# Kernel tuning notes

Measured on AMD Instinct MI355X. Metric: run time of the kernel, lower is better.

The kernel has to match this reference:

```python
import jax, jax.numpy as jnp
import numpy as np

B, N, K = 4, 4096, 16
D_POINTS, D_MODEL = 64, 256


def _ln(x, g, b, eps=1e-5):
    mu = jnp.mean(x, axis=-1, keepdims=True)
    var = jnp.mean((x - mu) ** 2, axis=-1, keepdims=True)
    return (x - mu) * jax.lax.rsqrt(var + eps) * g + b


def _gather(points, idx):
    # points: [B,N,C], idx: [B,N,K] -> [B,N,K,C]
    b = jnp.arange(points.shape[0])[:, None, None]
    return points[b, idx]


def setup_inputs() -> dict:
    key = jax.random.key(0)
    ks = jax.random.split(key, 16)
    std_qkv = np.sqrt(2.0 / D_MODEL).astype(np.float32)
    return {
        "xyz": jax.random.normal(ks[0], (B, N, 3), jnp.float32),
        "features": jax.random.normal(ks[1], (B, N, D_POINTS), jnp.float32),
        "W_pre": jax.random.normal(ks[2], (D_MODEL, D_POINTS), jnp.float32) * 0.02,
        "b_pre": jnp.zeros((D_MODEL,), jnp.float32),
        "W_post": jax.random.normal(ks[3], (D_POINTS, D_MODEL), jnp.float32) * 0.02,
        "b_post": jnp.zeros((D_POINTS,), jnp.float32),
        "Wp1": jax.random.normal(ks[4], (D_MODEL, 3), jnp.float32) * 0.02,
        "Wp2": jax.random.normal(ks[5], (D_MODEL, D_MODEL), jnp.float32) * 0.02,
        "Wa1": jax.random.normal(ks[6], (D_MODEL, D_MODEL), jnp.float32) * 0.02,
        "Wa2": jax.random.normal(ks[7], (D_MODEL, D_MODEL), jnp.float32) * 0.02,
        "WQ": jax.random.normal(ks[8], (D_MODEL, D_MODEL), jnp.float32) * std_qkv,
        "WK": jax.random.normal(ks[9], (D_MODEL, D_MODEL), jnp.float32) * std_qkv,
        "WV": jax.random.normal(ks[10], (D_MODEL, D_MODEL), jnp.float32) * std_qkv,
        "Wproj": jax.random.normal(ks[11], (D_MODEL, D_MODEL), jnp.float32) * 0.02,
        "g_dm": jnp.ones((D_MODEL,), jnp.float32),
        "b_dm": jnp.zeros((D_MODEL,), jnp.float32),
        "g_dp": jnp.ones((D_POINTS,), jnp.float32),
        "b_dp": jnp.zeros((D_POINTS,), jnp.float32),
    }


def reference(xyz, features, W_pre, b_pre, W_post, b_post, Wp1, Wp2, Wa1, Wa2,
              WQ, WK, WV, Wproj, g_dm, b_dm, g_dp, b_dp):
    # kNN (state == 'l'): pairwise squared distances, k smallest per point
    dists = jnp.sum((xyz[:, :, None, :] - xyz[:, None, :, :]) ** 2, axis=-1)  # [B,N,N]
    _, idx = jax.lax.top_k(-dists, K)  # [B,N,K] smallest distances (incl. self)

    knn_xyz = _gather(xyz, idx)                      # [B,N,K,3]
    inp = features @ W_pre.T + b_pre                 # [B,N,D]

    q = _ln(inp @ WQ.T, g_dm, b_dm)                  # [B,N,D]
    k_ = _gather(_ln(inp @ WK.T, g_dm, b_dm), idx)   # [B,N,K,D]
    v_ = _gather(_ln(inp @ WV.T, g_dm, b_dm), idx)   # [B,N,K,D]

    rel = xyz[:, :, None, :] - knn_xyz               # [B,N,K,3]
    pos = jax.nn.relu(rel @ Wp1.T) @ Wp2.T           # [B,N,K,D]

    attn = jax.nn.relu((q[:, :, None, :] - k_ + pos) @ Wa1.T) @ Wa2.T  # [B,N,K,D]
    attn = jax.nn.softmax(attn / jnp.sqrt(jnp.float32(D_MODEL)), axis=-2)

    res = jnp.einsum('bnkf,bnkf->bnf', attn, v_ + pos)  # vector attention reduce
    res = _ln(res @ Wproj.T, g_dm, b_dm)
    res = _ln(res @ W_post.T + b_post, g_dp, b_dp) + features
    return res
```

## Files before the change

### kernel.cpp

```cpp
#include <hip/hip_runtime.h>
#include <hip/hip_bf16.h>

typedef unsigned short u16;
typedef unsigned int   u32;
typedef __attribute__((ext_vector_type(8))) short bf16x8;
typedef __attribute__((ext_vector_type(4))) float f32x4;

#define MFMA16(a,b,c) __builtin_amdgcn_mfma_f32_16x16x32_bf16((a),(b),(c),0,0,0)

__device__ __forceinline__ float b2f(u32 h){ return __uint_as_float(h<<16); }
__device__ __forceinline__ u16 f2b(float f){
  u32 u = __float_as_uint(f);
  return (u16)((u + 0x7FFFu + ((u>>16)&1u))>>16);
}
__device__ __forceinline__ u32 pk2f(float a,float b){
  __hip_bfloat162 h = __float22bfloat162_rn(float2{a,b});
  return *reinterpret_cast<u32*>(&h);
}
__device__ __forceinline__ u32 umin32(u32 a,u32 b){ return a<b?a:b; }
__device__ __forceinline__ u32 umax32(u32 a,u32 b){ return a>b?a:b; }

template<int CTRL>
__device__ __forceinline__ float dpp_add(float x){
  int t = __builtin_amdgcn_update_dpp(0, __float_as_int(x), CTRL, 0xF, 0xF, true);
  return x + __int_as_float(t);
}
__device__ __forceinline__ float rowsum16(float x){
  x = dpp_add<0x121>(x);
  x = dpp_add<0x122>(x);
  x = dpp_add<0x124>(x);
  x = dpp_add<0x128>(x);
  return x;
}

__device__ __forceinline__ void async_copy16(const void* g, void* l){
  __builtin_amdgcn_global_load_lds((const __attribute__((address_space(1))) u32*)g,
                                   (__attribute__((address_space(3))) u32*)l, 16, 0, 0);
}

#define OFF_IDX    0ull
#define OFF_WQKV   3178496ull
#define OFF_WA1    3571712ull
#define OFF_WA2    3702784ull
#define OFF_WP2    3833856ull
#define OFF_WPROJ  3964928ull
#define OFF_WPOST  4096000ull
#define OFF_MCOMB  4128768ull
#define OFF_INP    4259840ull
#define OFF_LNQKV  37814272ull
#define OFF_QA     62980096ull
#define OFF_KA     71368704ull
#define OFF_RES    79757312ull
#define OFF_D1     88145920ull
#define WS_NEED    104923136ull
#define OFF_WP1PK  OFF_D1

__device__ __forceinline__ void ins16(u32 (&a)[16], u32 key){
  #pragma unroll
  for (int j = 15; j >= 1; --j){
    u32 r;
    asm("v_med3_u32 %0, %1, %2, %3" : "=v"(r) : "v"(a[j-1]), "v"(key), "v"(a[j]));
    a[j] = r;
  }
  a[0] = umin32(a[0], key);
}

__device__ __forceinline__ float dist2(float ax,float ay,float az,float bx,float by,float bz){
  const float dx = ax-bx, dy = ay-by, dz = az-bz;
  return __fmaf_rn(dx,dx, __fmaf_rn(dy,dy, dz*dz));
}

__global__ __launch_bounds__(256,2) void prep_w_k(
    const float* __restrict__ feat,
    const float* __restrict__ wpre, const float* __restrict__ bpre,
    const float* __restrict__ wq, const float* __restrict__ wk, const float* __restrict__ wv,
    const float* __restrict__ wa1, const float* __restrict__ wa2, const float* __restrict__ wp2,
    const float* __restrict__ wproj, const float* __restrict__ wpost,
    const float* __restrict__ wp1,
    u16* __restrict__ dwqkv, u16* __restrict__ dwa1, u16* __restrict__ dwa2,
    u16* __restrict__ dwp2, u16* __restrict__ dwproj, u16* __restrict__ dwpost,
    u16* __restrict__ dwp1pk, u16* __restrict__ dmcomb,
    u16* __restrict__ dinp){
  __shared__ __attribute__((aligned(16))) char smem[36864];
  const int bid = blockIdx.x, tid = threadIdx.x;
  if (bid < 1856){
    int id = bid*256 + tid;
    const float* s; u16* d; int off;
    if      (id <  65536){ s=wq;    d=dwqkv;        off=id; }
    else if (id < 131072){ s=wk;    d=dwqkv+65536;  off=id-65536; }
    else if (id < 196608){ s=wv;    d=dwqkv+131072; off=id-131072; }
    else if (id < 262144){ s=wa1;   d=dwa1;         off=id-196608; }
    else if (id < 327680){ s=wa2;   d=dwa2;         off=id-262144; }
    else if (id < 393216){ s=wp2;   d=dwp2;         off=id-327680; }
    else if (id < 458752){ s=wproj; d=dwproj;       off=id-393216; }
    else                 { s=wpost; d=dwpost;       off=id-458752; }
    d[off] = f2b(s[off]);
  } else if (bid == 1856){
    const int h = tid;
    const float w0 = wp1[h*3], w1 = wp1[h*3+1], w2 = wp1[h*3+2];
    uint4 a; a.x = pk2f(w0,w1); a.y = pk2f(w2,0.f); a.z = 0u; a.w = 0u;
    uint4 z; z.x = z.y = z.z = z.w = 0u;
    *(uint4*)&dwp1pk[h*32]    = a;
    *(uint4*)&dwp1pk[h*32+8]  = z;
    *(uint4*)&dwp1pk[h*32+16] = z;
    *(uint4*)&dwp1pk[h*32+24] = z;
  } else if (bid < 2113){
    const int f = bid - 1857, h = tid;
    float acc = 0.f;
    #pragma unroll 4
    for (int j = 0; j < 256; ++j) acc = __fmaf_rn(wa1[f*256+j], wp2[j*256+h], acc);
    dmcomb[f*256+h] = f2b(acc);
  } else {
    u16* As = (u16*)smem;
    u16* Bs = (u16*)smem + 9216;
    const int tb = bid - 2113;
    const int mb = tb >> 1, nb = tb & 1;
    #pragma unroll
    for (int i = 0; i < 32; ++i){
      const int e = i*256 + tid;
      const int row = e >> 6, k = e & 63;
      As[row*72+k] = f2b(feat[(size_t)(mb*128)*64 + e]);
      Bs[row*72+k] = f2b(wpre[(size_t)(nb*128)*64 + e]);
    }
    __syncthreads();
    const int lane = tid & 63, w = tid >> 6;
    const int mrow = lane & 15, quad = lane >> 4;
    const int wr = (w&1)*64, wc = (w>>1)*64;
    f32x4 acc[4][4];
    #pragma unroll
    for (int i=0;i<4;++i)
      #pragma unroll
      for (int j=0;j<4;++j)
        #pragma unroll
        for (int r=0;r<4;++r) acc[i][j][r] = 0.f;
    #pragma unroll
    for (int ks = 0; ks < 2; ++ks){
      const int koff = ks*32 + quad*8;
      bf16x8 af[4], bf[4];
      #pragma unroll
      for (int rt=0;rt<4;++rt) af[rt] = *(const bf16x8*)&As[(wr+rt*16+mrow)*72 + koff];
      #pragma unroll
      for (int ct=0;ct<4;++ct) bf[ct] = *(const bf16x8*)&Bs[(wc+ct*16+mrow)*72 + koff];
      #pragma unroll
      for (int rt=0;rt<4;++rt)
        #pragma unroll
        for (int ct=0;ct<4;++ct) acc[rt][ct] = MFMA16(af[rt], bf[ct], acc[rt][ct]);
    }
    #pragma unroll
    for (int rt=0;rt<4;++rt)
      #pragma unroll
      for (int ct=0;ct<4;++ct){
        const size_t row0 = (size_t)mb*128 + wr + rt*16 + quad*4;
        const int col = nb*128 + wc + ct*16 + mrow;
        const float bv = bpre[col];
        #pragma unroll
        for (int r=0;r<4;++r) dinp[(row0+r)*256 + col] = f2b(acc[rt][ct][r] + bv);
      }
  }
}

__global__ __launch_bounds__(256,2) void knn_k(
    const float* __restrict__ xyz, int* __restrict__ idxout){
  __shared__ __attribute__((aligned(16))) char smem[51200];
  float* sx = (float*)smem;
  float* sy = sx + 4160;
  float* sz = sy + 4160;
  int* lcnt   = (int*)(smem + 49920);
  int* tcnt   = (int*)(smem + 49984);
  u32* tbuf   = (u32*)(smem + 50048);
  int* tiebuf = (int*)(smem + 50112);
  const int bid = blockIdx.x, tid = threadIdx.x;
  const int b  = bid >> 8;
  const int n0 = (bid & 255) << 4;
  const float* base = xyz + (size_t)b*12288;
  #pragma unroll
  for (int i = 0; i < 12; ++i){
    const float4 v = *(const float4*)(base + tid*48 + i*4);
    const float vv[4] = {v.x, v.y, v.z, v.w};
    #pragma unroll
    for (int j = 0; j < 4; ++j){
      const int e = i*4 + j;
      const int c = e % 3;
      const int m = tid*16 + e/3;
      float* arr = (c==0)?sx:((c==1)?sy:sz);
      arr[(m>>8)*260 + (m&255)] = vv[j];
    }
  }
  if (tid < 16){ lcnt[tid] = 0; tcnt[tid] = 0; }
  __syncthreads();
  const int qi = tid >> 4, p = tid & 15;
  const int n = n0 + qi;
  const float qx = sx[(n>>8)*260 + (n&255)];
  const float qy = sy[(n>>8)*260 + (n&255)];
  const float qz = sz[(n>>8)*260 + (n&255)];
  u32 a[16];
  #pragma unroll
  for (int j = 0; j < 16; ++j) a[j] = 0xFFFFFFFFu;
  const float* px = sx + p*260;
  const float* py = sy + p*260;
  const float* pz = sz + p*260;
  #pragma unroll 2
  for (int i4 = 0; i4 < 64; ++i4){
    const float4 x4 = *(const float4*)(px + i4*4);
    const float4 y4 = *(const float4*)(py + i4*4);
    const float4 z4 = *(const float4*)(pz + i4*4);
    ins16(a, __float_as_uint(dist2(x4.x,y4.x,z4.x,qx,qy,qz)));
    ins16(a, __float_as_uint(dist2(x4.y,y4.y,z4.y,qx,qy,qz)));
    ins16(a, __float_as_uint(dist2(x4.z,y4.z,z4.z,qx,qy,qz)));
    ins16(a, __float_as_uint(dist2(x4.w,y4.w,z4.w,qx,qy,qz)));
  }
  #pragma unroll
  for (int s = 8; s >= 1; s >>= 1){
    u32 o[16];
    #pragma unroll
    for (int j = 0; j < 16; ++j) o[j] = __shfl_down(a[j], (unsigned)s, 64);
    if (p < s){
      #pragma unroll
      for (int j = 0; j < 16; ++j) ins16(a, o[j]);
    }
  }
  if (p == 0) tbuf[qi] = a[15];
  __syncthreads();
  const u32 T = tbuf[qi];
  int* orow = idxout + ((size_t)(b<<12)+n)*16;
  const int gbase = p*256;
  for (int i4 = 0; i4 < 64; ++i4){
    const float4 x4 = *(const float4*)(px + i4*4);
    const float4 y4 = *(const float4*)(py + i4*4);
    const float4 z4 = *(const float4*)(pz + i4*4);
    const float xv[4] = {x4.x,x4.y,x4.z,x4.w};
    const float yv[4] = {y4.x,y4.y,y4.z,y4.w};
    const float zv[4] = {z4.x,z4.y,z4.z,z4.w};
    #pragma unroll
    for (int j = 0; j < 4; ++j){
      const float d2 = dist2(xv[j],yv[j],zv[j],qx,qy,qz);
      const u32 kb = __float_as_uint(d2);
      if (kb < T){
        const int pos = atomicAdd(&lcnt[qi],1);
        if (pos < 16) orow[pos] = gbase + i4*4 + j;
      } else if (kb == T){
        const int t = atomicAdd(&tcnt[qi],1);
        if (t < 16) tiebuf[qi*16+t] = gbase + i4*4 + j;
      }
    }
  }
  __syncthreads();
  if (p == 0){
    int L = lcnt[qi]; if (L > 16) L = 16;
    int tc = tcnt[qi]; if (tc > 16) tc = 16;
    const int need = 16 - L;
    for (int r = 0; r < need; ++r){
      int best = 0x7FFFFFFF, bj = -1;
      for (int j = 0; j < tc; ++j){
        const int v = tiebuf[qi*16+j];
        if (v < best){ best = v; bj = j; }
      }
      if (bj >= 0){ tiebuf[qi*16+bj] = 0x7FFFFFFF; orow[L+r] = best; }
      else orow[L+r] = n;
    }
  }
}

#define LNP 264
__global__ __launch_bounds__(512,2) void gemmlnqa_k(
    const u16* __restrict__ inp, const u16* __restrict__ wqkv, const u16* __restrict__ wa1,
    u16* __restrict__ qa, u16* __restrict__ ka, u16* __restrict__ lnqkv,
    const float* __restrict__ g, const float* __restrict__ bta){
  __shared__ __attribute__((aligned(16))) u16 As[64*32];
  __shared__ __attribute__((aligned(16))) u16 Bs[256*32];
  __shared__ __attribute__((aligned(16))) u16 lnbuf[64*LNP];
  __shared__ float sS[64], sSS[64];
  const int z = blockIdx.z;
  const u16* wsel = wqkv + z*65536;
  const int tid = threadIdx.x, lane = tid & 63, w = tid >> 6;
  const int mrow = lane & 15, quad = lane >> 4;
  const size_t mbase = (size_t)blockIdx.x*64;
  const int wr = (w&1)*32, wc = (w>>1)*64;
  if (tid < 64){ sS[tid] = 0.f; sSS[tid] = 0.f; }
  f32x4 acc[2][4];
  #pragma unroll
  for (int i=0;i<2;++i)
    #pragma unroll
    for (int j=0;j<4;++j)
      #pragma unroll
      for (int r=0;r<4;++r) acc[i][j][r] = 0.f;
  const int sr = tid >> 2, sk = (tid & 3)*8;
  for (int k0 = 0; k0 < 256; k0 += 32){
    __syncthreads();
    if (tid < 256) async_copy16(inp + (mbase + sr)*256 + k0 + sk, &As[w*512]);
    async_copy16(wsel + (size_t)sr*256       + k0 + sk, &Bs[w*512]);
    async_copy16(wsel + (size_t)(128+sr)*256 + k0 + sk, &Bs[4096 + w*512]);
    __syncthreads();
    bf16x8 af[2], bf[4];
    #pragma unroll
    for (int rt=0;rt<2;++rt) af[rt] = *(const bf16x8*)&As[(wr+rt*16+mrow)*32 + quad*8];
    #pragma unroll
    for (int ct=0;ct<4;++ct) bf[ct] = *(const bf16x8*)&Bs[(wc+ct*16+mrow)*32 + quad*8];
    #pragma unroll
    for (int rt=0;rt<2;++rt)
      #pragma unroll
      for (int ct=0;ct<4;++ct) acc[rt][ct] = MFMA16(af[rt], bf[ct], acc[rt][ct]);
  }
  #pragma unroll
  for (int rt=0;rt<2;++rt)
    #pragma unroll
    for (int r=0;r<4;++r){
      float s  = acc[rt][0][r]+acc[rt][1][r]+acc[rt][2][r]+acc[rt][3][r];
      float ss = acc[rt][0][r]*acc[rt][0][r]+acc[rt][1][r]*acc[rt][1][r]
               + acc[rt][2][r]*acc[rt][2][r]+acc[rt][3][r]*acc[rt][3][r];
      s  = rowsum16(s);
      ss = rowsum16(ss);
      if (mrow == 0){
        const int row = wr + rt*16 + quad*4 + r;
        atomicAdd(&sS[row],  s);
        atomicAdd(&sSS[row], ss);
      }
    }
  __syncthreads();
  #pragma unroll
  for (int ct=0;ct<4;++ct){
    const int col = wc + ct*16 + mrow;
    const float gv = g[col], bv = bta[col];
    #pragma unroll
    for (int rt=0;rt<2;++rt)
      #pragma unroll
      for (int r=0;r<4;++r){
        const int row = wr + rt*16 + quad*4 + r;
        const float mu = sS[row]*(1.f/256.f);
        const float var = sSS[row]*(1.f/256.f) - mu*mu;
        const float rs = rsqrtf(var + 1e-5f);
        const u16 hv = f2b((acc[rt][ct][r]-mu)*rs*gv + bv);
        if (z == 2) lnqkv[(mbase+row)*768 + 512 + col] = hv;
        else        lnbuf[row*LNP + col] = hv;
      }
  }
  if (z == 2) return;
  u16* outp = (z == 0) ? qa : ka;
  f32x4 ac2[2][4];
  #pragma unroll
  for (int i=0;i<2;++i)
    #pragma unroll
    for (int j=0;j<4;++j)
      #pragma unroll
      for (int r=0;r<4;++r) ac2[i][j][r] = 0.f;
  for (int k0 = 0; k0 < 256; k0 += 32){
    __syncthreads();
    async_copy16(wa1 + (size_t)sr*256       + k0 + sk, &Bs[w*512]);
    async_copy16(wa1 + (size_t)(128+sr)*256 + k0 + sk, &Bs[4096 + w*512]);
    __syncthreads();
    bf16x8 af[2], bf[4];
    #pragma unroll
    for (int rt=0;rt<2;++rt) af[rt] = *(const bf16x8*)&lnbuf[(wr+rt*16+mrow)*LNP + k0 + quad*8];
    #pragma unroll
    for (int ct=0;ct<4;++ct) bf[ct] = *(const bf16x8*)&Bs[(wc+ct*16+mrow)*32 + quad*8];
    #pragma unroll
    for (int rt=0;rt<2;++rt)
      #pragma unroll
      for (int ct=0;ct<4;++ct) ac2[rt][ct] = MFMA16(af[rt], bf[ct], ac2[rt][ct]);
  }
  #pragma unroll
  for (int rt=0;rt<2;++rt)
    #pragma unroll
    for (int ct=0;ct<4;++ct){
      const size_t row0 = mbase + wr + rt*16 + quad*4;
      const int col = wc + ct*16 + mrow;
      #pragma unroll
      for (int r=0;r<4;++r) outp[(row0+r)*256 + col] = f2b(ac2[rt][ct][r]);
    }
}

__global__ __launch_bounds__(512,2) void projpost_k(
    const u16* __restrict__ res, const u16* __restrict__ wproj, const u16* __restrict__ wpost,
    const float* __restrict__ bpost,
    const float* __restrict__ g_dm, const float* __restrict__ b_dm,
    const float* __restrict__ g_dp, const float* __restrict__ b_dp,
    const float* __restrict__ feat, float* __restrict__ out){
  __shared__ __attribute__((aligned(16))) u16 As[64*32];
  __shared__ __attribute__((aligned(16))) u16 Bs[256*32];
  __shared__ __attribute__((aligned(16))) u16 lnbuf[64*LNP];
  __shared__ float sS[64], sSS[64], sS2[64], sSS2[64];
  const int tid = threadIdx.x, lane = tid & 63, w = tid >> 6;
  const int mrow = lane & 15, quad = lane >> 4;
  const size_t mbase = (size_t)blockIdx.x*64;
  const int wr = (w&1)*32, wc = (w>>1)*64;
  if (tid < 64){ sS[tid]=0.f; sSS[tid]=0.f; sS2[tid]=0.f; sSS2[tid]=0.f; }
  f32x4 acc[2][4];
  #pragma unroll
  for (int i=0;i<2;++i)
    #pragma unroll
    for (int j=0;j<4;++j)
      #pragma unroll
      for (int r=0;r<4;++r) acc[i][j][r] = 0.f;
  const int sr = tid >> 2, sk = (tid & 3)*8;
  for (int k0 = 0; k0 < 256; k0 += 32){
    __syncthreads();
    if (tid < 256) async_copy16(res + (mbase + sr)*256 + k0 + sk, &As[w*512]);
    async_copy16(wproj + (size_t)sr*256       + k0 + sk, &Bs[w*512]);
    async_copy16(wproj + (size_t)(128+sr)*256 + k0 + sk, &Bs[4096 + w*512]);
    __syncthreads();
    bf16x8 af[2], bf[4];
    #pragma unroll
    for (int rt=0;rt<2;++rt) af[rt] = *(const bf16x8*)&As[(wr+rt*16+mrow)*32 + quad*8];
    #pragma unroll
    for (int ct=0;ct<4;++ct) bf[ct] = *(const bf16x8*)&Bs[(wc+ct*16+mrow)*32 + quad*8];
    #pragma unroll
    for (int rt=0;rt<2;++rt)
      #pragma unroll
      for (int ct=0;ct<4;++ct) acc[rt][ct] = MFMA16(af[rt], bf[ct], acc[rt][ct]);
  }
  #pragma unroll
  for (int rt=0;rt<2;++rt)
    #pragma unroll
    for (int r=0;r<4;++r){
      float s  = acc[rt][0][r]+acc[rt][1][r]+acc[rt][2][r]+acc[rt][3][r];
      float ss = acc[rt][0][r]*acc[rt][0][r]+acc[rt][1][r]*acc[rt][1][r]
               + acc[rt][2][r]*acc[rt][2][r]+acc[rt][3][r]*acc[rt][3][r];
      s  = rowsum16(s);
      ss = rowsum16(ss);
      if (mrow == 0){
        const int row = wr + rt*16 + quad*4 + r;
        atomicAdd(&sS[row],  s);
        atomicAdd(&sSS[row], ss);
      }
    }
  __syncthreads();
  #pragma unroll
  for (int ct=0;ct<4;++ct){
    const int col = wc + ct*16 + mrow;
    const float gv = g_dm[col], bv = b_dm[col];
    #pragma unroll
    for (int rt=0;rt<2;++rt)
      #pragma unroll
      for (int r=0;r<4;++r){
        const int row = wr + rt*16 + quad*4 + r;
        const float mu = sS[row]*(1.f/256.f);
        const float var = sSS[row]*(1.f/256.f) - mu*mu;
        const float rs = rsqrtf(var + 1e-5f);
        lnbuf[row*LNP + col] = f2b((acc[rt][ct][r]-mu)*rs*gv + bv);
      }
  }
  const int wr2 = (w & 3)*16, wc2 = (w >> 2)*32;
  f32x4 ac2[2];
  #pragma unroll
  for (int j=0;j<2;++j)
    #pragma unroll
    for (int r=0;r<4;++r) ac2[j][r] = 0.f;
  for (int k0 = 0; k0 < 256; k0 += 32){
    __syncthreads();
    if (tid < 256) async_copy16(wpost + (size_t)sr*256 + k0 + sk, &Bs[w*512]);
    __syncthreads();
    bf16x8 af, bf[2];
    af = *(const bf16x8*)&lnbuf[(wr2+mrow)*LNP + k0 + quad*8];
    #pragma unroll
    for (int ct=0;ct<2;++ct) bf[ct] = *(const bf16x8*)&Bs[(wc2+ct*16+mrow)*32 + quad*8];
    #pragma unroll
    for (int ct=0;ct<2;++ct) ac2[ct] = MFMA16(af, bf[ct], ac2[ct]);
  }
  #pragma unroll
  for (int ct=0;ct<2;++ct){
    const float bv = bpost[wc2 + ct*16 + mrow];
    #pragma unroll
    for (int r=0;r<4;++r) ac2[ct][r] += bv;
  }
  #pragma unroll
  for (int r=0;r<4;++r){
    float s  = ac2[0][r] + ac2[1][r];
    float ss = ac2[0][r]*ac2[0][r] + ac2[1][r]*ac2[1][r];
    s  = rowsum16(s);
    ss = rowsum16(ss);
    if (mrow == 0){
      const int row = wr2 + quad*4 + r;
      atomicAdd(&sS2[row],  s);
      atomicAdd(&sSS2[row], ss);
    }
  }
  __syncthreads();
  #pragma unroll
  for (int ct=0;ct<2;++ct){
    const int col = wc2 + ct*16 + mrow;
    const float gv = g_dp[col], bv = b_dp[col];
    #pragma unroll
    for (int r=0;r<4;++r){
      const int row = wr2 + quad*4 + r;
      const float mu = sS2[row]*(1.f/64.f);
      const float var = sSS2[row]*(1.f/64.f) - mu*mu;
      const float rs = rsqrtf(var + 1e-5f);
      const size_t grow = mbase + row;
      out[grow*64 + col] = (ac2[ct][r]-mu)*rs*gv + bv + feat[grow*64 + col];
    }
  }
}

#define RELP 40
__device__ __forceinline__ u16* swzp(u16* p, int row, int cb){
  return (u16*)((char*)p + row*512 + (cb ^ ((row & 7) << 4)));
}
__global__ __launch_bounds__(1024,4) void attn_k(
    const float* __restrict__ xyz, const int* __restrict__ idxb,
    const u16* __restrict__ lnqkv, const u16* __restrict__ qa, const u16* __restrict__ ka,
    const u16* __restrict__ mcomb, const u16* __restrict__ wp2, const u16* __restrict__ wa2,
    const u16* __restrict__ wp1pk, u16* __restrict__ res){
  __shared__ __attribute__((aligned(16))) u16 h1buf[128*256];
  __shared__ __attribute__((aligned(16))) u16 h2buf[128*256];
  __shared__ __attribute__((aligned(16))) u16 qbuf[8*256];
  __shared__ __attribute__((aligned(16))) u16 srel[128*RELP];
  __shared__ int sidx[128];
  const int tid = threadIdx.x;
  const int b = blockIdx.x >> 9;
  const int nbase = (blockIdx.x & 511) << 3;
  const size_t gb = (size_t)b << 12;
  if (tid < 128){
    const int m = tid;
    const int im = idxb[(gb + nbase + (m>>4))*16 + (m&15)] & 4095;
    sidx[m] = im;
    const int nn = nbase + (m>>4);
    const float* pq = xyz + (gb+nn)*3;
    const float* pm = xyz + (gb+im)*3;
    const float rx = pq[0]-pm[0], ry = pq[1]-pm[1], rz = pq[2]-pm[2];
    uint4 a; a.x = pk2f(rx,ry); a.y = pk2f(rz,0.f); a.z = 0u; a.w = 0u;
    uint4 z; z.x = z.y = z.z = z.w = 0u;
    *(uint4*)&srel[m*RELP]    = a;
    *(uint4*)&srel[m*RELP+8]  = z;
    *(uint4*)&srel[m*RELP+16] = z;
    *(uint4*)&srel[m*RELP+24] = z;
  }
  __syncthreads();
  const int lane = tid & 63, w = tid >> 6;
  const int mrow = lane & 15, quad = lane >> 4;
  const int fr = w << 4;
  const int swc      = (mrow & 7) << 4;
  const int cbst     = (2*(fr + quad*4)) ^ swc;
  char* h1st = (char*)h1buf + mrow*512 + cbst;
  char* h2st = (char*)h2buf + mrow*512 + cbst;
  const int quadoff  = (quad*16) ^ (swc & 0x30);
  const char* h1rd = (const char*)h1buf + mrow*512 + quadoff;
  const char* h2rd = (const char*)h2buf + mrow*512 + quadoff;
  const int ksxc = swc & 0x40;
  {
    bf16x8 aW = *(const bf16x8*)&wp1pk[(fr+mrow)*32 + quad*8];
    #pragma unroll
    for (int mt=0;mt<8;++mt){
      bf16x8 bR = *(const bf16x8*)&srel[(mt*16+mrow)*RELP + quad*8];
      f32x4 hz;
      #pragma unroll
      for (int r=0;r<4;++r) hz[r]=0.f;
      hz = MFMA16(aW, bR, hz);
      float h0 = hz[0]>0.f?hz[0]:0.f, h1v = hz[1]>0.f?hz[1]:0.f;
      float h2v = hz[2]>0.f?hz[2]:0.f, h3 = hz[3]>0.f?hz[3]:0.f;
      uint2 o; o.x = pk2f(h0,h1v); o.y = pk2f(h2v,h3);
      *(uint2*)(h1st + mt*8192) = o;
    }
  }
  __syncthreads();
  {
    #pragma unroll
    for (int i = 0; i < 4; ++i){
      const int row = w*8 + i*2 + (lane>>5);
      const int c   = ((lane&31)*8) ^ ((row & 7) << 3);
      async_copy16(ka + (gb + (size_t)sidx[row])*256 + c,
                   &h2buf[w*2048 + i*512]);
    }
    if (w < 4){
      const int row = w*2 + (lane>>5);
      async_copy16(qa + (gb + nbase + row)*256 + (lane&31)*8, &qbuf[w*512]);
    }
  }
  f32x4 at[8], av[8];
  #pragma unroll
  for (int j=0;j<8;++j)
    #pragma unroll
    for (int r=0;r<4;++r){ at[j][r]=0.f; av[j][r]=0.f; }
  #pragma unroll 1
  for (int ks = 0; ks < 8; ++ks){
    const int koff = ks*32 + quad*8;
    bf16x8 aM = *(const bf16x8*)&mcomb[(fr+mrow)*256 + koff];
    bf16x8 aP = *(const bf16x8*)&wp2  [(fr+mrow)*256 + koff];
    const char* hb = h1rd + ((ks*64) ^ ksxc);
    #pragma unroll
    for (int mh=0; mh<2; ++mh){
      bf16x8 bH[4];
      #pragma unroll
      for (int mi=0;mi<4;++mi) bH[mi] = *(const bf16x8*)(hb + (mh*4+mi)*8192);
      #pragma unroll
      for (int mi=0;mi<4;++mi){
        at[mh*4+mi] = MFMA16(aM, bH[mi], at[mh*4+mi]);
        av[mh*4+mi] = MFMA16(bH[mi], aP, av[mh*4+mi]);
      }
    }
  }
  __syncthreads();
  #pragma unroll
  for (int mt=0;mt<8;++mt){
    u16* addr = (u16*)(h2st + mt*8192);
    const uint2 kv = *(const uint2*)addr;
    const uint2 qv = *(const uint2*)&qbuf[mt*256 + fr + quad*4];
    float t0 = at[mt][0] + b2f(qv.x&0xffff) - b2f(kv.x&0xffff);
    float t1 = at[mt][1] + b2f(qv.x>>16)    - b2f(kv.x>>16);
    float t2 = at[mt][2] + b2f(qv.y&0xffff) - b2f(kv.y&0xffff);
    float t3 = at[mt][3] + b2f(qv.y>>16)    - b2f(kv.y>>16);
    t0 = t0>0.f?t0:0.f; t1 = t1>0.f?t1:0.f; t2 = t2>0.f?t2:0.f; t3 = t3>0.f?t3:0.f;
    uint2 o; o.x = pk2f(t0,t1); o.y = pk2f(t2,t3);
    *(uint2*)addr = o;
  }
  __syncthreads();
  {
    #pragma unroll
    for (int i = 0; i < 4; ++i){
      const int row = w*8 + i*2 + (lane>>5);
      const int c   = ((lane&31)*8) ^ ((row & 7) << 3);
      async_copy16(lnqkv + (gb + (size_t)sidx[row])*768 + 512 + c,
                   &h1buf[w*2048 + i*512]);
    }
  }
  f32x4 al[8];
  #pragma unroll
  for (int j=0;j<8;++j)
    #pragma unroll
    for (int r=0;r<4;++r) al[j][r]=0.f;
  #pragma unroll 1
  for (int ks = 0; ks < 8; ++ks){
    const int koff = ks*32 + quad*8;
    bf16x8 aW = *(const bf16x8*)&wa2[(fr+mrow)*256 + koff];
    const char* hb = h2rd + ((ks*64) ^ ksxc);
    #pragma unroll
    for (int mh=0; mh<2; ++mh){
      bf16x8 bH[4];
      #pragma unroll
      for (int mi=0;mi<4;++mi) bH[mi] = *(const bf16x8*)(hb + (mh*4+mi)*8192);
      #pragma unroll
      for (int mi=0;mi<4;++mi) al[mh*4+mi] = MFMA16(bH[mi], aW, al[mh*4+mi]);
    }
  }
  __syncthreads();
  const float sc = 0.0901684f;
  const char* vb0 = (const char*)h1buf + (quad*4+0)*512 + ((2*(fr+mrow)) ^ ((((quad*4)+0)&7)<<4));
  const char* vb1 = (const char*)h1buf + (quad*4+1)*512 + ((2*(fr+mrow)) ^ ((((quad*4)+1)&7)<<4));
  const char* vb2 = (const char*)h1buf + (quad*4+2)*512 + ((2*(fr+mrow)) ^ ((((quad*4)+2)&7)<<4));
  const char* vb3 = (const char*)h1buf + (quad*4+3)*512 + ((2*(fr+mrow)) ^ ((((quad*4)+3)&7)<<4));
  #pragma unroll
  for (int mt=0;mt<8;++mt){
    float prs = 0.f, wgs = 0.f;
    {
      const float val = av[mt][0] + b2f(*(const u16*)(vb0 + mt*8192));
      const float pr = exp2f(al[mt][0]*sc); prs += pr; wgs += pr*val;
    }
    {
      const float val = av[mt][1] + b2f(*(const u16*)(vb1 + mt*8192));
      const float pr = exp2f(al[mt][1]*sc); prs += pr; wgs += pr*val;
    }
    {
      const float val = av[mt][2] + b2f(*(const u16*)(vb2 + mt*8192));
      const float pr = exp2f(al[mt][2]*sc); prs += pr; wgs += pr*val;
    }
    {
      const float val = av[mt][3] + b2f(*(const u16*)(vb3 + mt*8192));
      const float pr = exp2f(al[mt][3]*sc); prs += pr; wgs += pr*val;
    }
    prs += __shfl_xor(prs, 16, 64); prs += __shfl_xor(prs, 32, 64);
    wgs += __shfl_xor(wgs, 16, 64); wgs += __shfl_xor(wgs, 32, 64);
    const float rv = wgs * __builtin_amdgcn_rcpf(prs);
    if (quad == 0)
      res[(gb + nbase + mt)*256 + fr + mrow] = f2b(rv);
  }
}

extern "C" void kernel_launch(void* const* d_in, const int* in_sizes, int n_in,
                              void* d_out, int out_size, void* d_ws, size_t ws_size,
                              hipStream_t stream){
  const float* xyz    = (const float*)d_in[0];
  const float* feat   = (const float*)d_in[1];
  const float* W_pre  = (const float*)d_in[2];
  const float* b_pre  = (const float*)d_in[3];
  const float* W_post = (const float*)d_in[4];
  const float* b_post = (const float*)d_in[5];
  const float* Wp1    = (const float*)d_in[6];
  const float* Wp2    = (const float*)d_in[7];
  const float* Wa1    = (const float*)d_in[8];
  const float* Wa2    = (const float*)d_in[9];
  const float* WQ     = (const float*)d_in[10];
  const float* WK     = (const float*)d_in[11];
  const float* WV     = (const float*)d_in[12];
  const float* Wproj  = (const float*)d_in[13];
  const float* g_dm   = (const float*)d_in[14];
  const float* b_dm   = (const float*)d_in[15];
  const float* g_dp   = (const float*)d_in[16];
  const float* b_dp   = (const float*)d_in[17];
  float* out = (float*)d_out;
  if (ws_size < WS_NEED) return;
  char* ws = (char*)d_ws;
  int* idxw   = (int*)(ws + OFF_IDX);
  u16* wqkvb  = (u16*)(ws + OFF_WQKV);
  u16* wa1b   = (u16*)(ws + OFF_WA1);
  u16* wa2b   = (u16*)(ws + OFF_WA2);
  u16* wp2b   = (u16*)(ws + OFF_WP2);
  u16* wprojb = (u16*)(ws + OFF_WPROJ);
  u16* wpostb = (u16*)(ws + OFF_WPOST);
  u16* mcombb = (u16*)(ws + OFF_MCOMB);
  u16* inp    = (u16*)(ws + OFF_INP);
  u16* lnqkv  = (u16*)(ws + OFF_LNQKV);
  u16* qab    = (u16*)(ws + OFF_QA);
  u16* kab    = (u16*)(ws + OFF_KA);
  u16* resb   = (u16*)(ws + OFF_RES);
  u16* wp1pk  = (u16*)(ws + OFF_WP1PK);

  prep_w_k<<<2369,256,0,stream>>>(feat, W_pre, b_pre, WQ, WK, WV, Wa1, Wa2, Wp2,
                                  Wproj, W_post, Wp1,
                                  wqkvb, wa1b, wa2b, wp2b, wprojb, wpostb,
                                  wp1pk, mcombb, inp);
  knn_k<<<1024,256,0,stream>>>(xyz, idxw);
  gemmlnqa_k<<<dim3(256,1,3),512,0,stream>>>(inp, wqkvb, wa1b, qab, kab, lnqkv, g_dm, b_dm);
  attn_k<<<2048,1024,0,stream>>>(xyz,idxw,lnqkv,qab,kab,mcombb,wp2b,wa2b,wp1pk,resb);
  projpost_k<<<256,512,0,stream>>>(resb, wprojb, wpostb, b_post, g_dm, b_dm, g_dp, b_dp,
                                   feat, out);
}
```

Before: 392.4 us.

## Fuse kNN kernel into QKV GEMM launch as extra grid slices

Merges the kNN search kernel and the QKV GEMM+LayerNorm kernel into a single launch. Grid x selects either one of three GEMM projections or one of four kNN tile groups, so independent work runs concurrently. kNN blocks now run with 512 threads of which only 256 do work, and shared memory is a union sized for both paths. This saves one launch and lets the two stages overlap, but it wastes half the kNN threads and may lower kNN occupancy.

```diff
diff --git a/kernel.cpp b/kernel.cpp
--- a/kernel.cpp
+++ b/kernel.cpp
@@ -159,122 +159,134 @@
   }
 }
 
-__global__ __launch_bounds__(256,2) void knn_k(
-    const float* __restrict__ xyz, int* __restrict__ idxout){
-  __shared__ __attribute__((aligned(16))) char smem[51200];
-  float* sx = (float*)smem;
-  float* sy = sx + 4160;
-  float* sz = sy + 4160;
-  int* lcnt   = (int*)(smem + 49920);
-  int* tcnt   = (int*)(smem + 49984);
-  u32* tbuf   = (u32*)(smem + 50048);
-  int* tiebuf = (int*)(smem + 50112);
-  const int bid = blockIdx.x, tid = threadIdx.x;
-  const int b  = bid >> 8;
-  const int n0 = (bid & 255) << 4;
-  const float* base = xyz + (size_t)b*12288;
-  #pragma unroll
-  for (int i = 0; i < 12; ++i){
-    const float4 v = *(const float4*)(base + tid*48 + i*4);
-    const float vv[4] = {v.x, v.y, v.z, v.w};
-    #pragma unroll
-    for (int j = 0; j < 4; ++j){
-      const int e = i*4 + j;
-      const int c = e % 3;
-      const int m = tid*16 + e/3;
-      float* arr = (c==0)?sx:((c==1)?sy:sz);
-      arr[(m>>8)*260 + (m&255)] = vv[j];
-    }
-  }
-  if (tid < 16){ lcnt[tid] = 0; tcnt[tid] = 0; }
-  __syncthreads();
-  const int qi = tid >> 4, p = tid & 15;
-  const int n = n0 + qi;
-  const float qx = sx[(n>>8)*260 + (n&255)];
-  const float qy = sy[(n>>8)*260 + (n&255)];
-  const float qz = sz[(n>>8)*260 + (n&255)];
-  u32 a[16];
-  #pragma unroll
-  for (int j = 0; j < 16; ++j) a[j] = 0xFFFFFFFFu;
-  const float* px = sx + p*260;
-  const float* py = sy + p*260;
-  const float* pz = sz + p*260;
-  #pragma unroll 2
-  for (int i4 = 0; i4 < 64; ++i4){
-    const float4 x4 = *(const float4*)(px + i4*4);
-    const float4 y4 = *(const float4*)(py + i4*4);
-    const float4 z4 = *(const float4*)(pz + i4*4);
-    ins16(a, __float_as_uint(dist2(x4.x,y4.x,z4.x,qx,qy,qz)));
-    ins16(a, __float_as_uint(dist2(x4.y,y4.y,z4.y,qx,qy,qz)));
-    ins16(a, __float_as_uint(dist2(x4.z,y4.z,z4.z,qx,qy,qz)));
-    ins16(a, __float_as_uint(dist2(x4.w,y4.w,z4.w,qx,qy,qz)));
-  }
-  #pragma unroll
-  for (int s = 8; s >= 1; s >>= 1){
-    u32 o[16];
-    #pragma unroll
-    for (int j = 0; j < 16; ++j) o[j] = __shfl_down(a[j], (unsigned)s, 64);
-    if (p < s){
-      #pragma unroll
-      for (int j = 0; j < 16; ++j) ins16(a, o[j]);
-    }
-  }
-  if (p == 0) tbuf[qi] = a[15];
-  __syncthreads();
-  const u32 T = tbuf[qi];
-  int* orow = idxout + ((size_t)(b<<12)+n)*16;
-  const int gbase = p*256;
-  for (int i4 = 0; i4 < 64; ++i4){
-    const float4 x4 = *(const float4*)(px + i4*4);
-    const float4 y4 = *(const float4*)(py + i4*4);
-    const float4 z4 = *(const float4*)(pz + i4*4);
-    const float xv[4] = {x4.x,x4.y,x4.z,x4.w};
-    const float yv[4] = {y4.x,y4.y,y4.z,y4.w};
-    const float zv[4] = {z4.x,z4.y,z4.z,z4.w};
-    #pragma unroll
-    for (int j = 0; j < 4; ++j){
-      const float d2 = dist2(xv[j],yv[j],zv[j],qx,qy,qz);
-      const u32 kb = __float_as_uint(d2);
-      if (kb < T){
-        const int pos = atomicAdd(&lcnt[qi],1);
-        if (pos < 16) orow[pos] = gbase + i4*4 + j;
-      } else if (kb == T){
-        const int t = atomicAdd(&tcnt[qi],1);
-        if (t < 16) tiebuf[qi*16+t] = gbase + i4*4 + j;
-      }
-    }
-  }
-  __syncthreads();
-  if (p == 0){
-    int L = lcnt[qi]; if (L > 16) L = 16;
-    int tc = tcnt[qi]; if (tc > 16) tc = 16;
-    const int need = 16 - L;
-    for (int r = 0; r < need; ++r){
-      int best = 0x7FFFFFFF, bj = -1;
-      for (int j = 0; j < tc; ++j){
-        const int v = tiebuf[qi*16+j];
-        if (v < best){ best = v; bj = j; }
-      }
-      if (bj >= 0){ tiebuf[qi*16+bj] = 0x7FFFFFFF; orow[L+r] = best; }
-      else orow[L+r] = n;
-    }
-  }
-}
-
 #define LNP 264
-__global__ __launch_bounds__(512,2) void gemmlnqa_k(
+__global__ __launch_bounds__(512,2) void gemmknn_k(
     const u16* __restrict__ inp, const u16* __restrict__ wqkv, const u16* __restrict__ wa1,
     u16* __restrict__ qa, u16* __restrict__ ka, u16* __restrict__ lnqkv,
-    const float* __restrict__ g, const float* __restrict__ bta){
-  __shared__ __attribute__((aligned(16))) u16 As[64*32];
-  __shared__ __attribute__((aligned(16))) u16 Bs[256*32];
-  __shared__ __attribute__((aligned(16))) u16 lnbuf[64*LNP];
-  __shared__ float sS[64], sSS[64];
-  const int z = blockIdx.z;
+    const float* __restrict__ g, const float* __restrict__ bta,
+    const float* __restrict__ xyz, int* __restrict__ idxout){
+  __shared__ __attribute__((aligned(16))) char smem[54784];
+  const int zsel = blockIdx.x;
+  const int xb   = blockIdx.z;
+  const int tid  = threadIdx.x;
+  if (zsel >= 3){
+    float* sx = (float*)smem;
+    float* sy = sx + 4160;
+    float* sz = sy + 4160;
+    int* lcnt   = (int*)(smem + 49920);
+    int* tcnt   = (int*)(smem + 49984);
+    u32* tbuf   = (u32*)(smem + 50048);
+    int* tiebuf = (int*)(smem + 50112);
+    const int tile = (zsel - 3)*256 + xb;
+    const int b  = tile >> 8;
+    const int n0 = (tile & 255) << 4;
+    const float* base = xyz + (size_t)b*12288;
+    if (tid < 256){
+      #pragma unroll
+      for (int i = 0; i < 12; ++i){
+        const float4 v = *(const float4*)(base + tid*48 + i*4);
+        const float vv[4] = {v.x, v.y, v.z, v.w};
+        #pragma unroll
+        for (int j = 0; j < 4; ++j){
+          const int e = i*4 + j;
+          const int c = e % 3;
+          const int m = tid*16 + e/3;
+          float* arr = (c==0)?sx:((c==1)?sy:sz);
+          arr[(m>>8)*260 + (m&255)] = vv[j];
+        }
+      }
+      if (tid < 16){ lcnt[tid] = 0; tcnt[tid] = 0; }
+    }
+    __syncthreads();
+    const int qi = (tid >> 4) & 15, p = tid & 15;
+    const int n = n0 + qi;
+    u32 a[16];
+    const float* px = sx + p*260;
+    const float* py = sy + p*260;
+    const float* pz = sz + p*260;
+    float qx = 0.f, qy = 0.f, qz = 0.f;
+    if (tid < 256){
+      qx = sx[(n>>8)*260 + (n&255)];
+      qy = sy[(n>>8)*260 + (n&255)];
+      qz = sz[(n>>8)*260 + (n&255)];
+      #pragma unroll
+      for (int j = 0; j < 16; ++j) a[j] = 0xFFFFFFFFu;
+      #pragma unroll 2
+      for (int i4 = 0; i4 < 64; ++i4){
+        const float4 x4 = *(const float4*)(px + i4*4);
+        const float4 y4 = *(const float4*)(py + i4*4);
+        const float4 z4 = *(const float4*)(pz + i4*4);
+        ins16(a, __float_as_uint(dist2(x4.x,y4.x,z4.x,qx,qy,qz)));
+        ins16(a, __float_as_uint(dist2(x4.y,y4.y,z4.y,qx,qy,qz)));
+        ins16(a, __float_as_uint(dist2(x4.z,y4.z,z4.z,qx,qy,qz)));
+        ins16(a, __float_as_uint(dist2(x4.w,y4.w,z4.w,qx,qy,qz)));
+      }
+      #pragma unroll
+      for (int s = 8; s >= 1; s >>= 1){
+        u32 o[16];
+        #pragma unroll
+        for (int j = 0; j < 16; ++j) o[j] = __shfl_down(a[j], (unsigned)s, 64);
+        if (p < s){
+          #pragma unroll
+          for (int j = 0; j < 16; ++j) ins16(a, o[j]);
+        }
+      }
+      if (p == 0) tbuf[qi] = a[15];
+    }
+    __syncthreads();
+    if (tid < 256){
+      const u32 T = tbuf[qi];
+      int* orow = idxout + ((size_t)(b<<12)+n)*16;
+      const int gbase = p*256;
+      for (int i4 = 0; i4 < 64; ++i4){
+        const float4 x4 = *(const float4*)(px + i4*4);
+        const float4 y4 = *(const float4*)(py + i4*4);
+        const float4 z4 = *(const float4*)(pz + i4*4);
+        const float xv[4] = {x4.x,x4.y,x4.z,x4.w};
+        const float yv[4] = {y4.x,y4.y,y4.z,y4.w};
+        const float zv[4] = {z4.x,z4.y,z4.z,z4.w};
+        #pragma unroll
+        for (int j = 0; j < 4; ++j){
+          const float d2 = dist2(xv[j],yv[j],zv[j],qx,qy,qz);
+          const u32 kb = __float_as_uint(d2);
+          if (kb < T){
+            const int pos = atomicAdd(&lcnt[qi],1);
+            if (pos < 16) orow[pos] = gbase + i4*4 + j;
+          } else if (kb == T){
+            const int t = atomicAdd(&tcnt[qi],1);
+            if (t < 16) tiebuf[qi*16+t] = gbase + i4*4 + j;
+          }
+        }
+      }
+    }
+    __syncthreads();
+    if (tid < 256 && p == 0){
+      int* orow = idxout + ((size_t)(b<<12)+n)*16;
+      int L = lcnt[qi]; if (L > 16) L = 16;
+      int tc = tcnt[qi]; if (tc > 16) tc = 16;
+      const int need = 16 - L;
+      for (int r = 0; r < need; ++r){
+        int best = 0x7FFFFFFF, bj = -1;
+        for (int j = 0; j < tc; ++j){
+          const int v = tiebuf[qi*16+j];
+          if (v < best){ best = v; bj = j; }
+        }
+        if (bj >= 0){ tiebuf[qi*16+bj] = 0x7FFFFFFF; orow[L+r] = best; }
+        else orow[L+r] = n;
+      }
+    }
+    return;
+  }
+  u16* As    = (u16*)smem;
+  u16* Bs    = (u16*)(smem + 4096);
+  u16* lnbuf = (u16*)(smem + 20480);
+  float* sS  = (float*)(smem + 54272);
+  float* sSS = (float*)(smem + 54528);
+  const int z = zsel;
   const u16* wsel = wqkv + z*65536;
-  const int tid = threadIdx.x, lane = tid & 63, w = tid >> 6;
+  const int lane = tid & 63, w = tid >> 6;
   const int mrow = lane & 15, quad = lane >> 4;
-  const size_t mbase = (size_t)blockIdx.x*64;
+  const size_t mbase = (size_t)xb*64;
   const int wr = (w&1)*32, wc = (w>>1)*64;
   if (tid < 64){ sS[tid] = 0.f; sSS[tid] = 0.f; }
   f32x4 acc[2][4];
@@ -707,8 +719,8 @@
                                   Wproj, W_post, Wp1,
                                   wqkvb, wa1b, wa2b, wp2b, wprojb, wpostb,
                                   wp1pk, mcombb, inp);
-  knn_k<<<1024,256,0,stream>>>(xyz, idxw);
-  gemmlnqa_k<<<dim3(256,1,3),512,0,stream>>>(inp, wqkvb, wa1b, qab, kab, lnqkv, g_dm, b_dm);
+  gemmknn_k<<<dim3(7,1,256),512,0,stream>>>(inp, wqkvb, wa1b, qab, kab, lnqkv,
+                                            g_dm, b_dm, xyz, idxw);
   attn_k<<<2048,1024,0,stream>>>(xyz,idxw,lnqkv,qab,kab,mcombb,wp2b,wa2b,wp1pk,resb);
   projpost_k<<<256,512,0,stream>>>(resb, wprojb, wpostb, b_post, g_dm, b_dm, g_dp, b_dp,
                                    feat, out);
```

Result: slower. 421.7 us (+7.5%).
